# Kernel tuning notes

Measured on AMD Instinct MI355X. Metric: run time of the kernel, lower is better.

The kernel has to match this reference:

```python
import jax, jax.numpy as jnp
import numpy as np

N_TBINS = 1024
K = 64
BETA = 100.0
SIGMA = 10.0
EPS = 1e-8
B = 16384


def _irf_kernel():
    # gaussian_pulse centered at (n-1)//2, circ_shifted: normalized and rolled so peak is at bin 0
    t = jnp.arange(N_TBINS, dtype=jnp.float32)
    mu = (N_TBINS - 1) // 2
    g = jnp.exp(-0.5 * ((t - mu) / SIGMA) ** 2)
    g = g / g.sum()
    return jnp.roll(g, -mu)


def _zero_norm(x, axis):
    xz = x - x.mean(axis=axis, keepdims=True)
    return xz / (jnp.linalg.norm(xz, axis=axis, keepdims=True) + EPS)


def setup_inputs() -> dict:
    key = jax.random.key(0)
    k1, k2, k3, k4, k5 = jax.random.split(key, 5)
    bins = jax.random.randint(k1, (B,), 0, N_TBINS)
    photon_counts = jax.random.uniform(k2, (B,), dtype=jnp.float32) * 1000.0 + 100.0
    sbrs = jax.random.uniform(k3, (B,), dtype=jnp.float32) * 5.0 + 0.1
    learnable_input = jnp.ones((N_TBINS, 1), dtype=jnp.float32)
    bound = float(np.sqrt(6.0 / N_TBINS))  # kaiming_uniform_ on (k, n_tbins, 1)
    cmat_weight = jax.random.uniform(k4, (K, N_TBINS), minval=-bound, maxval=bound, dtype=jnp.float32)
    noise_eps = jax.random.normal(k5, (B, N_TBINS), dtype=jnp.float32)
    return {"bins": bins, "photon_counts": photon_counts, "sbrs": sbrs,
            "learnable_input": learnable_input, "cmat_weight": cmat_weight,
            "noise_eps": noise_eps}


def reference(bins, photon_counts, sbrs, learnable_input, cmat_weight, noise_eps):
    x = jax.nn.relu(learnable_input[:, 0])                      # (n,)
    irf = _irf_kernel()
    irf_input = jnp.fft.irfft(jnp.fft.rfft(x) * jnp.fft.rfft(irf), n=N_TBINS)  # circular conv, (n,)
    amb_per_bin = photon_counts / sbrs / N_TBINS                # (B,)
    scaling = photon_counts / irf_input.sum()                   # (B,)
    shifts = bins % N_TBINS
    # torch.roll(v, s): out[t] = v[(t - s) % n]  -> batched gather instead of python loop
    idx = (jnp.arange(N_TBINS)[None, :] - shifts[:, None]) % N_TBINS  # (B, n)
    shifted = irf_input[idx]                                    # (B, n)
    scaled = shifted * scaling[:, None] + amb_per_bin[:, None]  # (B, n)
    noisy = scaled + jnp.sqrt(scaled) * noise_eps               # reparameterized N(0, sqrt(scaled))
    # Conv1d(in=n_tbins, out=k, ksize=1) on (B, n, 1) == matmul
    out = jnp.einsum('kc,bc->bk', cmat_weight, noisy)           # (B, k)
    input_norm = _zero_norm(out, axis=-1)                       # zero-norm over k
    corr_norm = _zero_norm(cmat_weight, axis=0)                 # (k, n), zero-norm over k
    zncc = jnp.einsum('bk,kn->bn', input_norm, corr_norm)       # (B, n)
    sm = jax.nn.softmax(BETA * zncc, axis=-1)
    pred_depths = jnp.sum(sm * jnp.arange(N_TBINS, dtype=jnp.float32), axis=-1)  # (B,)
    return zncc[..., None], pred_depths
```

## Files before the change

kernel.cpp:

```cpp
#include <hip/hip_runtime.h>
#include <math.h>


#define NT 1024

typedef unsigned short u16;
typedef short bf16x8 __attribute__((ext_vector_type(8)));
typedef float f32x4 __attribute__((ext_vector_type(4)));

__device__ __forceinline__ u16 f2bf(float f) {
  unsigned u = __float_as_uint(f);
  u = u + 0x7FFFu + ((u >> 16) & 1u);
  return (u16)(u >> 16);
}
__device__ __forceinline__ float bf2f(u16 h) {
  return __uint_as_float(((unsigned)h) << 16);
}

__global__ __launch_bounds__(1024) void prelude(const float* __restrict__ learn,
                                                const float* __restrict__ cmat,
                                                float* __restrict__ irf_input,
                                                float* __restrict__ S,
                                                u16* __restrict__ cmatH,
                                                u16* __restrict__ cmatL) {
  __shared__ float red[NT];
  __shared__ float irf_l[NT];
  __shared__ float x_l[NT];
  int t = threadIdx.x;
  float d = ((float)t - 511.0f) / 10.0f;
  float g = expf(-0.5f * d * d);
  red[t] = g;
  __syncthreads();
  for (int s = 512; s > 0; s >>= 1) {
    if (t < s) red[t] += red[t + s];
    __syncthreads();
  }
  float gsum = red[0];
  irf_l[(t - 511) & (NT - 1)] = g / gsum;
  x_l[t] = fmaxf(learn[t], 0.0f);
  __syncthreads();
  float acc = 0.0f;
  for (int dd = -96; dd <= 96; ++dd)
    acc += irf_l[dd & (NT - 1)] * x_l[(t - dd) & (NT - 1)];
  irf_input[t] = acc;
  red[t] = acc;
  __syncthreads();
  for (int s = 512; s > 0; s >>= 1) {
    if (t < s) red[t] += red[t + s];
    __syncthreads();
  }
  if (t == 0) S[0] = red[0];
  for (int j = 0; j < 64; ++j) {
    int idx = t + NT * j;
    float v = cmat[idx];
    u16 h = f2bf(v);
    cmatH[idx] = h;
    cmatL[idx] = f2bf(v - bf2f(h));
  }
}

__global__ __launch_bounds__(256) void corr_init(const float* __restrict__ cmat,
                                                 u16* __restrict__ corrTH,
                                                 u16* __restrict__ corrTL) {
  int lane = threadIdx.x & 63;
  int wv = threadIdx.x >> 6;
  int n = blockIdx.x * 4 + wv;
  float w = cmat[lane * NT + n];
  float s = w;
#pragma unroll
  for (int off = 32; off > 0; off >>= 1) s += __shfl_xor(s, off);
  float mean = s * (1.0f / 64.0f);
  float dd = w - mean;
  float q = dd * dd;
#pragma unroll
  for (int off = 32; off > 0; off >>= 1) q += __shfl_xor(q, off);
  float val = dd / (sqrtf(q) + 1e-8f);
  u16 h = f2bf(val);
  corrTH[n * 64 + lane] = h;
  corrTL[n * 64 + lane] = f2bf(val - bf2f(h));
}

__global__ __launch_bounds__(256, 2) void fused_main(const int* __restrict__ bins,
                                                     const float* __restrict__ photon,
                                                     const float* __restrict__ sbrs,
                                                     const float* __restrict__ noise,
                                                     const float* __restrict__ irfin,
                                                     const float* __restrict__ Sp,
                                                     const u16* __restrict__ cmatH,
                                                     const u16* __restrict__ cmatL,
                                                     const u16* __restrict__ corrTH,
                                                     const u16* __restrict__ corrTL,
                                                     float* __restrict__ zncc,
                                                     float* __restrict__ pred) {
  __shared__ float irf_s[NT];
  __shared__ u16 noisyH[16 * NT];
  __shared__ u16 noisyL[16 * NT];
  __shared__ float out_s[16][68];
  __shared__ u16 inormH[16 * 64];
  __shared__ u16 inormL[16 * 64];
  __shared__ float red_m[4][16];
  __shared__ float red_e[4][16];
  __shared__ float red_n[4][16];

  int tid = threadIdx.x;
  int lane = tid & 63, w = tid >> 6;
  int row = lane & 15, kg = lane >> 4;
  long b0 = (long)blockIdx.x * 16;

  for (int i = tid; i < NT; i += 256) irf_s[i] = irfin[i];
  __syncthreads();
  float S = Sp[0];

#pragma unroll 1
  for (int rr = 0; rr < 4; ++rr) {
    int r = w * 4 + rr;
    long b = b0 + r;
    int shift = bins[b] & (NT - 1);
    float ph = photon[b];
    float scal = ph / S;
    float amb = ph / sbrs[b] * (1.0f / 1024.0f);
    const float* nrow = noise + b * NT;
#pragma unroll
    for (int i = 0; i < 8; ++i) {
      int c0 = 2 * lane + 128 * i;
      float2 nz = *reinterpret_cast<const float2*>(nrow + c0);
      float sc0 = fmaf(irf_s[(c0 - shift) & (NT - 1)], scal, amb);
      float sc1 = fmaf(irf_s[(c0 + 1 - shift) & (NT - 1)], scal, amb);
      float v0 = fmaf(sqrtf(sc0), nz.x, sc0);
      float v1 = fmaf(sqrtf(sc1), nz.y, sc1);
      u16 h0 = f2bf(v0), h1 = f2bf(v1);
      u16 l0 = f2bf(v0 - bf2f(h0)), l1 = f2bf(v1 - bf2f(h1));
      int word = (r * 512 + lane + 64 * i) ^ ((r & 7) << 2);
      reinterpret_cast<unsigned*>(noisyH)[word] = (unsigned)h0 | ((unsigned)h1 << 16);
      reinterpret_cast<unsigned*>(noisyL)[word] = (unsigned)l0 | ((unsigned)l1 << 16);
    }
  }
  __syncthreads();

  {
    const u16* cHp = cmatH + (size_t)(16 * w + row) * NT + 8 * kg;
    const u16* cLp = cmatL + (size_t)(16 * w + row) * NT + 8 * kg;
    int aBase = row * 2048 + 16 * kg;
    int swz = (row & 7) << 4;
    f32x4 aHH = {0.f, 0.f, 0.f, 0.f}, aHL = aHH, aLH = aHH;
#pragma unroll 4
    for (int s = 0; s < 32; ++s) {
      int off = (aBase + 64 * s) ^ swz;
      bf16x8 ah = *reinterpret_cast<const bf16x8*>(reinterpret_cast<const char*>(noisyH) + off);
      bf16x8 al = *reinterpret_cast<const bf16x8*>(reinterpret_cast<const char*>(noisyL) + off);
      bf16x8 bh = *reinterpret_cast<const bf16x8*>(cHp + 32 * s);
      bf16x8 bl = *reinterpret_cast<const bf16x8*>(cLp + 32 * s);
      aHH = __builtin_amdgcn_mfma_f32_16x16x32_bf16(ah, bh, aHH, 0, 0, 0);
      aHL = __builtin_amdgcn_mfma_f32_16x16x32_bf16(ah, bl, aHL, 0, 0, 0);
      aLH = __builtin_amdgcn_mfma_f32_16x16x32_bf16(al, bh, aLH, 0, 0, 0);
    }
    f32x4 o = aHH + aHL + aLH;
#pragma unroll
    for (int q = 0; q < 4; ++q) out_s[4 * kg + q][16 * w + row] = o[q];
  }
  __syncthreads();

#pragma unroll
  for (int rr = 0; rr < 4; ++rr) {
    int r = w * 4 + rr;
    float v = out_s[r][lane];
    float s = v;
#pragma unroll
    for (int off = 32; off > 0; off >>= 1) s += __shfl_xor(s, off);
    float mean = s * (1.0f / 64.0f);
    float dd = v - mean;
    float q = dd * dd;
#pragma unroll
    for (int off = 32; off > 0; off >>= 1) q += __shfl_xor(q, off);
    float val = dd / (sqrtf(q) + 1e-8f);
    u16 h = f2bf(val);
    u16 lo = f2bf(val - bf2f(h));
    int boff = (r * 128 + lane * 2) ^ ((r & 7) << 4);
    *reinterpret_cast<u16*>(reinterpret_cast<char*>(inormH) + boff) = h;
    *reinterpret_cast<u16*>(reinterpret_cast<char*>(inormL) + boff) = lo;
  }
  __syncthreads();

  int swz = (row & 7) << 4;
  int a0 = (row * 128 + 16 * kg) ^ swz;
  int a1 = (row * 128 + 64 + 16 * kg) ^ swz;
  bf16x8 a2h0 = *reinterpret_cast<const bf16x8*>(reinterpret_cast<const char*>(inormH) + a0);
  bf16x8 a2h1 = *reinterpret_cast<const bf16x8*>(reinterpret_cast<const char*>(inormH) + a1);
  bf16x8 a2l0 = *reinterpret_cast<const bf16x8*>(reinterpret_cast<const char*>(inormL) + a0);
  bf16x8 a2l1 = *reinterpret_cast<const bf16x8*>(reinterpret_cast<const char*>(inormL) + a1);

  f32x4 acc2[16];
  f32x4 mx = {-INFINITY, -INFINITY, -INFINITY, -INFINITY};
#pragma unroll
  for (int j = 0; j < 16; ++j) {
    int n0 = 256 * w + 16 * j;
    const u16* pH = corrTH + (size_t)(n0 + row) * 64 + 8 * kg;
    const u16* pL = corrTL + (size_t)(n0 + row) * 64 + 8 * kg;
    bf16x8 b0h = *reinterpret_cast<const bf16x8*>(pH);
    bf16x8 b1h = *reinterpret_cast<const bf16x8*>(pH + 32);
    bf16x8 b0l = *reinterpret_cast<const bf16x8*>(pL);
    bf16x8 b1l = *reinterpret_cast<const bf16x8*>(pL + 32);
    f32x4 t1 = {0.f, 0.f, 0.f, 0.f}, t2 = t1, t3 = t1;
    t1 = __builtin_amdgcn_mfma_f32_16x16x32_bf16(a2h0, b0h, t1, 0, 0, 0);
    t2 = __builtin_amdgcn_mfma_f32_16x16x32_bf16(a2h0, b0l, t2, 0, 0, 0);
    t3 = __builtin_amdgcn_mfma_f32_16x16x32_bf16(a2l0, b0h, t3, 0, 0, 0);
    t1 = __builtin_amdgcn_mfma_f32_16x16x32_bf16(a2h1, b1h, t1, 0, 0, 0);
    t2 = __builtin_amdgcn_mfma_f32_16x16x32_bf16(a2h1, b1l, t2, 0, 0, 0);
    t3 = __builtin_amdgcn_mfma_f32_16x16x32_bf16(a2l1, b1h, t3, 0, 0, 0);
    f32x4 z = t1 + t2 + t3;
    acc2[j] = z;
#pragma unroll
    for (int q = 0; q < 4; ++q) {
      zncc[(b0 + 4 * kg + q) * NT + n0 + row] = z[q];
      mx[q] = fmaxf(mx[q], z[q]);
    }
  }

#pragma unroll
  for (int q = 0; q < 4; ++q) {
#pragma unroll
    for (int off = 1; off < 16; off <<= 1) mx[q] = fmaxf(mx[q], __shfl_xor(mx[q], off));
  }
  if (row == 0) {
#pragma unroll
    for (int q = 0; q < 4; ++q) red_m[w][4 * kg + q] = mx[q];
  }
  __syncthreads();
  f32x4 rm;
#pragma unroll
  for (int q = 0; q < 4; ++q)
    rm[q] = fmaxf(fmaxf(red_m[0][4 * kg + q], red_m[1][4 * kg + q]),
                  fmaxf(red_m[2][4 * kg + q], red_m[3][4 * kg + q]));

  f32x4 es = {0.f, 0.f, 0.f, 0.f}, ns = es;
#pragma unroll
  for (int j = 0; j < 16; ++j) {
    float nf = (float)(256 * w + 16 * j + row);
#pragma unroll
    for (int q = 0; q < 4; ++q) {
      float e = expf(100.0f * (acc2[j][q] - rm[q]));
      es[q] += e;
      ns[q] = fmaf(nf, e, ns[q]);
    }
  }
#pragma unroll
  for (int q = 0; q < 4; ++q) {
#pragma unroll
    for (int off = 1; off < 16; off <<= 1) {
      es[q] += __shfl_xor(es[q], off);
      ns[q] += __shfl_xor(ns[q], off);
    }
  }
  if (row == 0) {
#pragma unroll
    for (int q = 0; q < 4; ++q) { red_e[w][4 * kg + q] = es[q]; red_n[w][4 * kg + q] = ns[q]; }
  }
  __syncthreads();
  if (tid < 16) {
    float e = red_e[0][tid] + red_e[1][tid] + red_e[2][tid] + red_e[3][tid];
    float n = red_n[0][tid] + red_n[1][tid] + red_n[2][tid] + red_n[3][tid];
    pred[b0 + tid] = n / e;
  }
}

extern "C" void kernel_launch(void* const* d_in, const int* in_sizes, int n_in,
                              void* d_out, int out_size, void* d_ws, size_t ws_size,
                              hipStream_t stream) {
  const int*   bins   = (const int*)d_in[0];
  const float* photon = (const float*)d_in[1];
  const float* sbrs   = (const float*)d_in[2];
  const float* learn  = (const float*)d_in[3];
  const float* cmat   = (const float*)d_in[4];
  const float* noise  = (const float*)d_in[5];
  float* out = (float*)d_out;
  float* wsf = (float*)d_ws;

  float* irf_input = wsf;
  float* Sslot     = wsf + 1024;
  u16* cmatH  = (u16*)(wsf + 2048);
  u16* cmatL  = cmatH + 65536;
  u16* corrTH = cmatL + 65536;
  u16* corrTL = corrTH + 65536;

  int B = in_sizes[0];
  float* pred = out + (size_t)B * NT;

  hipLaunchKernelGGL(prelude, dim3(1), dim3(1024), 0, stream,
                     learn, cmat, irf_input, Sslot, cmatH, cmatL);
  hipLaunchKernelGGL(corr_init, dim3(256), dim3(256), 0, stream, cmat, corrTH, corrTL);
  hipLaunchKernelGGL(fused_main, dim3(B / 16), dim3(256), 0, stream,
                     bins, photon, sbrs, noise, irf_input, Sslot,
                     cmatH, cmatL, corrTH, corrTL, out, pred);
}
```

Measured before the change: 210.6 us.

## Build noisy MFMA operands in registers and split K across waves

The first GEMM no longer stages the 16x1024 noisy tile through shared memory. Each wave builds its bf16 hi/lo A-fragments directly in registers from the noise reads and accumulates over a quarter of the 1024-channel dimension for all 64 outputs. Partial sums are then reduced through a small shared buffer. This removes about 64 KB of LDS per block, so launch bounds rise to 4 blocks per SM. The prelude's bf16 split of cmat moves into the parallel corr_init kernel, the triple accumulators collapse into one chained accumulator, and softmax uses __expf, which slightly changes numerics.

```diff
diff --git a/kernel.cpp b/kernel.cpp
--- a/kernel.cpp
+++ b/kernel.cpp
@@ -18,11 +18,8 @@
 }
 
 __global__ __launch_bounds__(1024) void prelude(const float* __restrict__ learn,
-                                                const float* __restrict__ cmat,
                                                 float* __restrict__ irf_input,
-                                                float* __restrict__ S,
-                                                u16* __restrict__ cmatH,
-                                                u16* __restrict__ cmatL) {
+                                                float* __restrict__ S) {
   __shared__ float red[NT];
   __shared__ float irf_l[NT];
   __shared__ float x_l[NT];
@@ -50,20 +47,23 @@
     __syncthreads();
   }
   if (t == 0) S[0] = red[0];
-  for (int j = 0; j < 64; ++j) {
-    int idx = t + NT * j;
+}
+
+__global__ __launch_bounds__(256) void corr_init(const float* __restrict__ cmat,
+                                                 u16* __restrict__ corrTH,
+                                                 u16* __restrict__ corrTL,
+                                                 u16* __restrict__ cmatH,
+                                                 u16* __restrict__ cmatL) {
+  int tid = threadIdx.x;
+  {
+    int idx = blockIdx.x * 256 + tid;
     float v = cmat[idx];
     u16 h = f2bf(v);
     cmatH[idx] = h;
     cmatL[idx] = f2bf(v - bf2f(h));
   }
-}
-
-__global__ __launch_bounds__(256) void corr_init(const float* __restrict__ cmat,
-                                                 u16* __restrict__ corrTH,
-                                                 u16* __restrict__ corrTL) {
-  int lane = threadIdx.x & 63;
-  int wv = threadIdx.x >> 6;
+  int lane = tid & 63;
+  int wv = tid >> 6;
   int n = blockIdx.x * 4 + wv;
   float w = cmat[lane * NT + n];
   float s = w;
@@ -80,7 +80,7 @@
   corrTL[n * 64 + lane] = f2bf(val - bf2f(h));
 }
 
-__global__ __launch_bounds__(256, 2) void fused_main(const int* __restrict__ bins,
+__global__ __launch_bounds__(256, 4) void fused_main(const int* __restrict__ bins,
                                                      const float* __restrict__ photon,
                                                      const float* __restrict__ sbrs,
                                                      const float* __restrict__ noise,
@@ -93,9 +93,7 @@
                                                      float* __restrict__ zncc,
                                                      float* __restrict__ pred) {
   __shared__ float irf_s[NT];
-  __shared__ u16 noisyH[16 * NT];
-  __shared__ u16 noisyL[16 * NT];
-  __shared__ float out_s[16][68];
+  __shared__ float part[4][16][68];
   __shared__ u16 inormH[16 * 64];
   __shared__ u16 inormL[16 * 64];
   __shared__ float red_m[4][16];
@@ -106,64 +104,61 @@
   int lane = tid & 63, w = tid >> 6;
   int row = lane & 15, kg = lane >> 4;
   long b0 = (long)blockIdx.x * 16;
+  long b = b0 + row;
+
+  int shift = bins[b] & (NT - 1);
+  float ph = photon[b];
+  float sb = sbrs[b];
 
   for (int i = tid; i < NT; i += 256) irf_s[i] = irfin[i];
   __syncthreads();
   float S = Sp[0];
-
-#pragma unroll 1
+  float scal = ph / S;
+  float amb = ph / sb * (1.0f / 1024.0f);
+  const float* nrow = noise + b * NT + w * 256;
+
+  f32x4 acc[4];
+#pragma unroll
+  for (int t = 0; t < 4; ++t) acc[t] = (f32x4){0.f, 0.f, 0.f, 0.f};
+
+#pragma unroll 2
+  for (int s = 0; s < 8; ++s) {
+    int c = 8 * kg + 32 * s;
+    int cabs = w * 256 + c;
+    float4 nz0 = *reinterpret_cast<const float4*>(nrow + c);
+    float4 nz1 = *reinterpret_cast<const float4*>(nrow + c + 4);
+    float nzv[8] = {nz0.x, nz0.y, nz0.z, nz0.w, nz1.x, nz1.y, nz1.z, nz1.w};
+    bf16x8 ah, al;
+#pragma unroll
+    for (int e = 0; e < 8; ++e) {
+      float sc = fmaf(irf_s[(cabs + e - shift) & (NT - 1)], scal, amb);
+      float v = fmaf(sqrtf(sc), nzv[e], sc);
+      u16 h = f2bf(v);
+      ah[e] = (short)h;
+      al[e] = (short)f2bf(v - bf2f(h));
+    }
+#pragma unroll
+    for (int t = 0; t < 4; ++t) {
+      const u16* pH = cmatH + (size_t)(16 * t + row) * NT + cabs;
+      const u16* pL = cmatL + (size_t)(16 * t + row) * NT + cabs;
+      bf16x8 bh = *reinterpret_cast<const bf16x8*>(pH);
+      bf16x8 bl = *reinterpret_cast<const bf16x8*>(pL);
+      acc[t] = __builtin_amdgcn_mfma_f32_16x16x32_bf16(al, bh, acc[t], 0, 0, 0);
+      acc[t] = __builtin_amdgcn_mfma_f32_16x16x32_bf16(ah, bl, acc[t], 0, 0, 0);
+      acc[t] = __builtin_amdgcn_mfma_f32_16x16x32_bf16(ah, bh, acc[t], 0, 0, 0);
+    }
+  }
+#pragma unroll
+  for (int t = 0; t < 4; ++t)
+#pragma unroll
+    for (int q = 0; q < 4; ++q) part[w][4 * kg + q][16 * t + row] = acc[t][q];
+  __syncthreads();
+
+#pragma unroll
   for (int rr = 0; rr < 4; ++rr) {
     int r = w * 4 + rr;
-    long b = b0 + r;
-    int shift = bins[b] & (NT - 1);
-    float ph = photon[b];
-    float scal = ph / S;
-    float amb = ph / sbrs[b] * (1.0f / 1024.0f);
-    const float* nrow = noise + b * NT;
-#pragma unroll
-    for (int i = 0; i < 8; ++i) {
-      int c0 = 2 * lane + 128 * i;
-      float2 nz = *reinterpret_cast<const float2*>(nrow + c0);
-      float sc0 = fmaf(irf_s[(c0 - shift) & (NT - 1)], scal, amb);
-      float sc1 = fmaf(irf_s[(c0 + 1 - shift) & (NT - 1)], scal, amb);
-      float v0 = fmaf(sqrtf(sc0), nz.x, sc0);
-      float v1 = fmaf(sqrtf(sc1), nz.y, sc1);
-      u16 h0 = f2bf(v0), h1 = f2bf(v1);
-      u16 l0 = f2bf(v0 - bf2f(h0)), l1 = f2bf(v1 - bf2f(h1));
-      int word = (r * 512 + lane + 64 * i) ^ ((r & 7) << 2);
-      reinterpret_cast<unsigned*>(noisyH)[word] = (unsigned)h0 | ((unsigned)h1 << 16);
-      reinterpret_cast<unsigned*>(noisyL)[word] = (unsigned)l0 | ((unsigned)l1 << 16);
-    }
-  }
-  __syncthreads();
-
-  {
-    const u16* cHp = cmatH + (size_t)(16 * w + row) * NT + 8 * kg;
-    const u16* cLp = cmatL + (size_t)(16 * w + row) * NT + 8 * kg;
-    int aBase = row * 2048 + 16 * kg;
-    int swz = (row & 7) << 4;
-    f32x4 aHH = {0.f, 0.f, 0.f, 0.f}, aHL = aHH, aLH = aHH;
-#pragma unroll 4
-    for (int s = 0; s < 32; ++s) {
-      int off = (aBase + 64 * s) ^ swz;
-      bf16x8 ah = *reinterpret_cast<const bf16x8*>(reinterpret_cast<const char*>(noisyH) + off);
-      bf16x8 al = *reinterpret_cast<const bf16x8*>(reinterpret_cast<const char*>(noisyL) + off);
-      bf16x8 bh = *reinterpret_cast<const bf16x8*>(cHp + 32 * s);
-      bf16x8 bl = *reinterpret_cast<const bf16x8*>(cLp + 32 * s);
-      aHH = __builtin_amdgcn_mfma_f32_16x16x32_bf16(ah, bh, aHH, 0, 0, 0);
-      aHL = __builtin_amdgcn_mfma_f32_16x16x32_bf16(ah, bl, aHL, 0, 0, 0);
-      aLH = __builtin_amdgcn_mfma_f32_16x16x32_bf16(al, bh, aLH, 0, 0, 0);
-    }
-    f32x4 o = aHH + aHL + aLH;
-#pragma unroll
-    for (int q = 0; q < 4; ++q) out_s[4 * kg + q][16 * w + row] = o[q];
-  }
-  __syncthreads();
-
-#pragma unroll
-  for (int rr = 0; rr < 4; ++rr) {
-    int r = w * 4 + rr;
-    float v = out_s[r][lane];
+    float v = part[0][r][lane] + part[1][r][lane] +
+              part[2][r][lane] + part[3][r][lane];
     float s = v;
 #pragma unroll
     for (int off = 32; off > 0; off >>= 1) s += __shfl_xor(s, off);
@@ -200,14 +195,13 @@
     bf16x8 b1h = *reinterpret_cast<const bf16x8*>(pH + 32);
     bf16x8 b0l = *reinterpret_cast<const bf16x8*>(pL);
     bf16x8 b1l = *reinterpret_cast<const bf16x8*>(pL + 32);
-    f32x4 t1 = {0.f, 0.f, 0.f, 0.f}, t2 = t1, t3 = t1;
-    t1 = __builtin_amdgcn_mfma_f32_16x16x32_bf16(a2h0, b0h, t1, 0, 0, 0);
-    t2 = __builtin_amdgcn_mfma_f32_16x16x32_bf16(a2h0, b0l, t2, 0, 0, 0);
-    t3 = __builtin_amdgcn_mfma_f32_16x16x32_bf16(a2l0, b0h, t3, 0, 0, 0);
-    t1 = __builtin_amdgcn_mfma_f32_16x16x32_bf16(a2h1, b1h, t1, 0, 0, 0);
-    t2 = __builtin_amdgcn_mfma_f32_16x16x32_bf16(a2h1, b1l, t2, 0, 0, 0);
-    t3 = __builtin_amdgcn_mfma_f32_16x16x32_bf16(a2l1, b1h, t3, 0, 0, 0);
-    f32x4 z = t1 + t2 + t3;
+    f32x4 z = {0.f, 0.f, 0.f, 0.f};
+    z = __builtin_amdgcn_mfma_f32_16x16x32_bf16(a2l0, b0h, z, 0, 0, 0);
+    z = __builtin_amdgcn_mfma_f32_16x16x32_bf16(a2h0, b0l, z, 0, 0, 0);
+    z = __builtin_amdgcn_mfma_f32_16x16x32_bf16(a2h0, b0h, z, 0, 0, 0);
+    z = __builtin_amdgcn_mfma_f32_16x16x32_bf16(a2l1, b1h, z, 0, 0, 0);
+    z = __builtin_amdgcn_mfma_f32_16x16x32_bf16(a2h1, b1l, z, 0, 0, 0);
+    z = __builtin_amdgcn_mfma_f32_16x16x32_bf16(a2h1, b1h, z, 0, 0, 0);
     acc2[j] = z;
 #pragma unroll
     for (int q = 0; q < 4; ++q) {
@@ -238,7 +232,7 @@
     float nf = (float)(256 * w + 16 * j + row);
 #pragma unroll
     for (int q = 0; q < 4; ++q) {
-      float e = expf(100.0f * (acc2[j][q] - rm[q]));
+      float e = __expf(100.0f * (acc2[j][q] - rm[q]));
       es[q] += e;
       ns[q] = fmaf(nf, e, ns[q]);
     }
@@ -285,9 +279,9 @@
   int B = in_sizes[0];
   float* pred = out + (size_t)B * NT;
 
-  hipLaunchKernelGGL(prelude, dim3(1), dim3(1024), 0, stream,
-                     learn, cmat, irf_input, Sslot, cmatH, cmatL);
-  hipLaunchKernelGGL(corr_init, dim3(256), dim3(256), 0, stream, cmat, corrTH, corrTL);
+  hipLaunchKernelGGL(prelude, dim3(1), dim3(1024), 0, stream, learn, irf_input, Sslot);
+  hipLaunchKernelGGL(corr_init, dim3(256), dim3(256), 0, stream,
+                     cmat, corrTH, corrTL, cmatH, cmatL);
   hipLaunchKernelGGL(fused_main, dim3(B / 16), dim3(256), 0, stream,
                      bins, photon, sbrs, noise, irf_input, Sslot,
                      cmatH, cmatL, corrTH, corrTL, out, pred);
```

Result: faster. 190.2 us (-9.7%).
